# Performance work log

Hardware: AMD Instinct MI355X
Metric: run time of the kernel (lower is better)

## Reference

```python
import jax, jax.numpy as jnp
import numpy as np

TWO_PI = 6.283185307179586


def setup_inputs() -> dict:
    key = jax.random.key(0)
    k1, k2, k3, k4, k5, k6 = jax.random.split(key, 6)
    B, T, D = 2, 8192, 1024
    x = jax.random.normal(k1, (B, T, D), dtype=jnp.float32)
    # nn.Linear weights are [out, in]; init with small scale like torch default
    s = 1.0 / np.sqrt(D)
    Wk = jax.random.uniform(k2, (D, D), jnp.float32, -s, s)
    Wv = jax.random.uniform(k3, (D, D), jnp.float32, -s, s)
    Wo = jax.random.uniform(k4, (D, D), jnp.float32, -s, s)
    # random phasor frequencies in [0, 2*pi)
    freqs = jax.random.uniform(k5, (D,), jnp.float32, 0.0, TWO_PI)
    return {"x": x, "Wk": Wk, "Wv": Wv, "Wo": Wo, "freqs": freqs}


def reference(x, Wk, Wv, Wo, freqs):
    B, T, C = x.shape
    # k projection is computed in the original forward but never used downstream
    k_real = x @ Wk.T  # [B,T,D] (dead value, kept for fidelity)
    v_real = x @ Wv.T  # [B,T,D]
    v = v_real.astype(jnp.complex64)
    # rotors: per-position unit phasors exp(i * t * freqs), shape [T, D]
    t = jnp.arange(T, dtype=jnp.float32)
    rotors = jnp.exp(1j * (t[:, None] * freqs[None, :])).astype(jnp.complex64)
    # bind each value with its rotor and accumulate causally (O(N) memory trace)
    memory_trace = jnp.cumsum(v * rotors[None, :, :], axis=1)  # [B,T,D] complex64
    # retrieve by unbinding with the conjugate rotor; take the real component
    retrieved = jnp.real(memory_trace * jnp.conj(rotors)[None, :, :])  # [B,T,D]
    return retrieved @ Wo.T
```

## Files before the change

kernel.cpp:

```cpp
#include <hip/hip_runtime.h>
#include <hip/hip_bf16.h>


#define B_  2
#define T_  8192
#define D_  1024
#define BT_ 16384
#define CS_ 64
#define NCHUNK_ 128

typedef __attribute__((ext_vector_type(4))) float f32x4;
typedef __attribute__((ext_vector_type(8))) short bf16x8;

static __device__ inline unsigned short f2bf(float f) {
    union { float f; unsigned int u; } a;
    a.f = f;
    unsigned int u = a.u;
    return (unsigned short)((u + 0x7FFFu + ((u >> 16) & 1u)) >> 16);
}
static __device__ inline float bf2f(unsigned short h) {
    union { unsigned int u; float f; } a;
    a.u = ((unsigned int)h) << 16;
    return a.f;
}

__global__ __launch_bounds__(256) void cast_all(const float* __restrict__ x,
                                                const float* __restrict__ Wv,
                                                const float* __restrict__ Wo,
                                                unsigned short* __restrict__ xb,
                                                unsigned short* __restrict__ wvb,
                                                unsigned short* __restrict__ wob) {
    const int nx = BT_ * D_ / 4;
    const int nw = D_ * D_ / 4;
    int i = blockIdx.x * 256 + threadIdx.x;
    const float4* src;
    unsigned short* dst;
    int j;
    if (i < nx)            { src = (const float4*)x;  dst = xb;  j = i; }
    else if (i < nx + nw)  { src = (const float4*)Wv; dst = wvb; j = i - nx; }
    else                   { src = (const float4*)Wo; dst = wob; j = i - nx - nw; }
    float4 v = src[j];
    ushort4 o;
    o.x = f2bf(v.x); o.y = f2bf(v.y); o.z = f2bf(v.z); o.w = f2bf(v.w);
    ((ushort4*)dst)[j] = o;
}

template <bool BF16OUT, bool FUSE_SUMS>
__global__ __launch_bounds__(512, 2) void gemm_bt(const short* __restrict__ A,
                                                  const short* __restrict__ Bm,
                                                  void* __restrict__ Cout,
                                                  const float* __restrict__ freqs,
                                                  float* __restrict__ csum,
                                                  int M, int N, int K) {
    __shared__ short lds[65536];
    const int tid = threadIdx.x;
    const int lane = tid & 63;
    const int wave = tid >> 6;
    const int wm = wave >> 2, wn = wave & 3;

    const int nb = N >> 8;
    const int id = blockIdx.x;
    const int xcd = id & 7;
    const int slot = id >> 3;
    const int bn = (slot % nb) * 256;
    const int bm = (xcd * ((M >> 8) >> 3) + slot / nb) * 256;

    const int srow = lane >> 3;
    const int sg = lane & 7;
    const short* gsrc[8];
#pragma unroll
    for (int c = 0; c < 4; ++c) {
        const int r = c * 64 + wave * 8 + srow;
        const int col = (sg ^ (r & 7)) * 8;
        gsrc[c]     = A  + (size_t)(bm + r) * K + col;
        gsrc[c + 4] = Bm + (size_t)(bn + r) * K + col;
    }

    auto stage = [&](int kt, int sl) {
        const int koff = kt * 64;
        short* dstA = &lds[sl * 32768 + wave * 512];
        short* dstB = &lds[sl * 32768 + 16384 + wave * 512];
#pragma unroll
        for (int c = 0; c < 4; ++c) {
            __builtin_amdgcn_global_load_lds(
                (const __attribute__((address_space(1))) void*)(gsrc[c] + koff),
                (__attribute__((address_space(3))) void*)(dstA + c * 4096), 16, 0, 0);
            __builtin_amdgcn_global_load_lds(
                (const __attribute__((address_space(1))) void*)(gsrc[c + 4] + koff),
                (__attribute__((address_space(3))) void*)(dstB + c * 4096), 16, 0, 0);
        }
    };

    const int c4r = lane >> 4;
    int aoff[8][2], boff[4][2];
#pragma unroll
    for (int i = 0; i < 8; ++i) {
        const int m = wm * 128 + i * 16 + (lane & 15);
#pragma unroll
        for (int ks = 0; ks < 2; ++ks)
            aoff[i][ks] = m * 64 + (((ks * 4 + c4r) ^ (m & 7)) * 8);
    }
#pragma unroll
    for (int j = 0; j < 4; ++j) {
        const int n = wn * 64 + j * 16 + (lane & 15);
#pragma unroll
        for (int ks = 0; ks < 2; ++ks)
            boff[j][ks] = 16384 + n * 64 + (((ks * 4 + c4r) ^ (n & 7)) * 8);
    }

    f32x4 acc[8][4] = {};

    stage(0, 0);
    stage(1, 1);

    const int NT = K >> 6;
#pragma unroll 1
    for (int t = 0; t < NT; ++t) {
        if (t < NT - 1) asm volatile("s_waitcnt vmcnt(8)" ::: "memory");
        else            asm volatile("s_waitcnt vmcnt(0)" ::: "memory");
        __builtin_amdgcn_sched_barrier(0);
        __builtin_amdgcn_s_barrier();
        __builtin_amdgcn_sched_barrier(0);

        const int sb = (t & 1) * 32768;
#pragma unroll
        for (int ks = 0; ks < 2; ++ks) {
            bf16x8 bb[4];
#pragma unroll
            for (int j = 0; j < 4; ++j)
                bb[j] = *(const bf16x8*)&lds[sb + boff[j][ks]];
#pragma unroll
            for (int ih = 0; ih < 2; ++ih) {
                bf16x8 aa[4];
#pragma unroll
                for (int ii = 0; ii < 4; ++ii)
                    aa[ii] = *(const bf16x8*)&lds[sb + aoff[ih * 4 + ii][ks]];
                __builtin_amdgcn_s_setprio(1);
#pragma unroll
                for (int ii = 0; ii < 4; ++ii)
#pragma unroll
                    for (int j = 0; j < 4; ++j)
                        acc[ih * 4 + ii][j] = __builtin_amdgcn_mfma_f32_16x16x32_bf16(
                            aa[ii], bb[j], acc[ih * 4 + ii][j], 0, 0, 0);
                __builtin_amdgcn_s_setprio(0);
            }
        }
        asm volatile("s_waitcnt lgkmcnt(0)" ::: "memory");
        __builtin_amdgcn_sched_barrier(0);
        __builtin_amdgcn_s_barrier();
        __builtin_amdgcn_sched_barrier(0);
        if (t < NT - 2) stage(t + 2, t & 1);
    }

    const int row0 = c4r * 4;
#pragma unroll
    for (int i = 0; i < 8; ++i) {
#pragma unroll
        for (int j = 0; j < 4; ++j) {
            const int col = bn + wn * 64 + j * 16 + (lane & 15);
#pragma unroll
            for (int r = 0; r < 4; ++r) {
                const size_t row = (size_t)bm + wm * 128 + i * 16 + row0 + r;
                if constexpr (BF16OUT)
                    ((unsigned short*)Cout)[row * N + col] = f2bf(acc[i][j][r]);
                else
                    ((float*)Cout)[row * N + col] = acc[i][j][r];
            }
        }
    }

    if constexpr (FUSE_SUMS) {
        const int b = bm >> 13;
        const int trow = bm & 8191;
#pragma unroll
        for (int ig = 0; ig < 2; ++ig) {
            const int chunk = (trow >> 6) + wm * 2 + ig;
            const int t0 = trow + wm * 128 + ig * 64 + c4r * 4;
#pragma unroll
            for (int j = 0; j < 4; ++j) {
                const int d = bn + wn * 64 + j * 16 + (lane & 15);
                const float f = freqs[d];
                float ss, cc2;
                sincosf((float)t0 * f, &ss, &cc2);
                float s1, c1;
                sincosf(f, &s1, &c1);
                float c2 = c1 * c1 - s1 * s1, s2 = 2.f * c1 * s1;
                float c4 = c2 * c2 - s2 * s2, s4 = 2.f * c2 * s2;
                float c8 = c4 * c4 - s4 * s4, s8 = 2.f * c4 * s4;
                float c12 = c8 * c4 - s8 * s4, s12 = s8 * c4 + c8 * s4;
                float c13 = c12 * c1 - s12 * s1, s13 = s12 * c1 + c12 * s1;
                float ar = 0.f, ai = 0.f;
                float cr = cc2, sr2 = ss;
#pragma unroll
                for (int ii = 0; ii < 4; ++ii) {
                    const int i = ig * 4 + ii;
#pragma unroll
                    for (int r = 0; r < 4; ++r) {
                        const float w = acc[i][j][r];
                        ar = fmaf(w, cr, ar); ai = fmaf(w, sr2, ai);
                        const float ec = (r < 3) ? c1 : c13;
                        const float es = (r < 3) ? s1 : s13;
                        const float nc = cr * ec - sr2 * es;
                        const float ns = sr2 * ec + cr * es;
                        cr = nc; sr2 = ns;
                    }
                }
                ar += __shfl_xor(ar, 16); ai += __shfl_xor(ai, 16);
                ar += __shfl_xor(ar, 32); ai += __shfl_xor(ai, 32);
                if (c4r == 0)
                    *(float2*)(csum + (((size_t)b * NCHUNK_ + chunk) * D_ + d) * 2) =
                        make_float2(ar, ai);
            }
        }
    }
}

__global__ __launch_bounds__(256) void scan_pass2(float* __restrict__ csum) {
    const int g = blockIdx.x * 256 + threadIdx.x;
    const int b = g / D_;
    const int d = g % D_;
    float2* cs = (float2*)csum;
    const size_t base = (size_t)b * NCHUNK_ * D_ + d;
    float pr = 0.f, pi = 0.f;
    for (int cc = 0; cc < NCHUNK_; cc += 32) {
        float2 buf[32];
#pragma unroll
        for (int k = 0; k < 32; ++k) buf[k] = cs[base + (size_t)(cc + k) * D_];
#pragma unroll
        for (int k = 0; k < 32; ++k) {
            float r = buf[k].x, im = buf[k].y;
            buf[k] = make_float2(pr, pi);
            pr += r; pi += im;
        }
#pragma unroll
        for (int k = 0; k < 32; ++k) cs[base + (size_t)(cc + k) * D_] = buf[k];
    }
}

__global__ __launch_bounds__(256) void scan_pass3(const unsigned short* __restrict__ v,
                                                  const float* __restrict__ freqs,
                                                  const float* __restrict__ csum,
                                                  unsigned short* __restrict__ ret) {
    const int chunk = blockIdx.x;
    const int d0 = blockIdx.y * 512 + threadIdx.x * 2;
    const int b = blockIdx.z;

    float fr[2], s[2], c[2], sf[2], cf[2], ar[2], ai[2];
    {
        float2 f2 = *(const float2*)(freqs + d0);
        fr[0] = f2.x; fr[1] = f2.y;
    }
    const float t0f = (float)(chunk * CS_);
#pragma unroll
    for (int k = 0; k < 2; ++k) {
        sincosf(t0f * fr[k], &s[k], &c[k]);
        sincosf(fr[k], &sf[k], &cf[k]);
    }
    {
        const float4 o = *(const float4*)(csum + (((size_t)b * NCHUNK_ + chunk) * D_ + d0) * 2);
        ar[0] = o.x; ai[0] = o.y; ar[1] = o.z; ai[1] = o.w;
    }
    const unsigned int* vp = (const unsigned int*)(v + ((size_t)b * T_ + chunk * CS_) * D_ + d0);
    unsigned int* rp = (unsigned int*)(ret + ((size_t)b * T_ + chunk * CS_) * D_ + d0);
    for (int tb = 0; tb < CS_; tb += 8) {
        unsigned int w[8];
#pragma unroll
        for (int u = 0; u < 8; ++u) w[u] = vp[(size_t)(tb + u) * (D_ / 2)];
#pragma unroll
        for (int u = 0; u < 8; ++u) {
            float wv[2], o[2];
            wv[0] = bf2f((unsigned short)w[u]);
            wv[1] = bf2f((unsigned short)(w[u] >> 16));
#pragma unroll
            for (int k = 0; k < 2; ++k) {
                ar[k] = fmaf(wv[k], c[k], ar[k]);
                ai[k] = fmaf(wv[k], s[k], ai[k]);
                o[k] = ar[k] * c[k] + ai[k] * s[k];
                float nc = c[k] * cf[k] - s[k] * sf[k];
                float ns = s[k] * cf[k] + c[k] * sf[k];
                c[k] = nc; s[k] = ns;
            }
            rp[(size_t)(tb + u) * (D_ / 2)] =
                (unsigned int)f2bf(o[0]) | ((unsigned int)f2bf(o[1]) << 16);
        }
    }
}

extern "C" void kernel_launch(void* const* d_in, const int* in_sizes, int n_in,
                              void* d_out, int out_size, void* d_ws, size_t ws_size,
                              hipStream_t stream) {
    const float* x     = (const float*)d_in[0];
    const float* Wv    = (const float*)d_in[2];
    const float* Wo    = (const float*)d_in[3];
    const float* freqs = (const float*)d_in[4];
    float* out = (float*)d_out;

    char* ws = (char*)d_ws;
    unsigned short* x_bf  = (unsigned short*)ws;
    unsigned short* Wv_bf = (unsigned short*)(ws + 33554432);
    unsigned short* Wo_bf = (unsigned short*)(ws + 35651584);
    unsigned short* ret   = (unsigned short*)(ws + 37748736);
    float*          csum  = (float*)(ws + 71303168);
    unsigned short* v_bf = (unsigned short*)d_out;

    cast_all<<<(BT_ * D_ / 4 + 2 * D_ * D_ / 4) / 256, 256, 0, stream>>>(
        x, Wv, Wo, x_bf, Wv_bf, Wo_bf);

    gemm_bt<true, true><<<(BT_ / 256) * (D_ / 256), 512, 0, stream>>>(
        (const short*)x_bf, (const short*)Wv_bf, (void*)v_bf, freqs, csum, BT_, D_, D_);

    scan_pass2<<<(B_ * D_) / 256, 256, 0, stream>>>(csum);
    dim3 p3grid(NCHUNK_, D_ / 512, B_);
    scan_pass3<<<p3grid, 256, 0, stream>>>(v_bf, freqs, csum, ret);

    gemm_bt<false, false><<<(BT_ / 256) * (D_ / 256), 512, 0, stream>>>(
        (const short*)ret, (const short*)Wo_bf, (void*)out, nullptr, nullptr, BT_, D_, D_);
}
```

Before: 234.2 us.

## Split GEMM main loop into four quadrant phases with interleaved async loads

Restructures the bf16 MFMA GEMM main loop into four quadrant sub-phases. Each phase loads a subset of A/B fragments from LDS, issues a few global-to-LDS loads for future tiles, and runs 16 MFMAs. This spreads global loads across the iteration and overlaps LDS reads with MFMA work, instead of one big compute block followed by a batched stage. It also simplifies the address math with precomputed swizzle offsets, at the cost of more barriers per iteration and tricky buffer-reuse ordering.

```diff
diff --git a/kernel.cpp b/kernel.cpp
--- a/kernel.cpp
+++ b/kernel.cpp
@@ -67,89 +67,126 @@
 
     const int srow = lane >> 3;
     const int sg = lane & 7;
-    const short* gsrc[8];
-#pragma unroll
-    for (int c = 0; c < 4; ++c) {
-        const int r = c * 64 + wave * 8 + srow;
-        const int col = (sg ^ (r & 7)) * 8;
-        gsrc[c]     = A  + (size_t)(bm + r) * K + col;
-        gsrc[c + 4] = Bm + (size_t)(bn + r) * K + col;
-    }
-
-    auto stage = [&](int kt, int sl) {
-        const int koff = kt * 64;
-        short* dstA = &lds[sl * 32768 + wave * 512];
-        short* dstB = &lds[sl * 32768 + 16384 + wave * 512];
-#pragma unroll
-        for (int c = 0; c < 4; ++c) {
-            __builtin_amdgcn_global_load_lds(
-                (const __attribute__((address_space(1))) void*)(gsrc[c] + koff),
-                (__attribute__((address_space(3))) void*)(dstA + c * 4096), 16, 0, 0);
-            __builtin_amdgcn_global_load_lds(
-                (const __attribute__((address_space(1))) void*)(gsrc[c + 4] + koff),
-                (__attribute__((address_space(3))) void*)(dstB + c * 4096), 16, 0, 0);
-        }
+    const size_t cstep = (size_t)64 * K;
+    const short* gA = A + (size_t)(bm + wave * 8 + srow) * K + ((sg ^ srow) * 8);
+    const short* gB = Bm + (size_t)(bn + wave * 8 + srow) * K + ((sg ^ srow) * 8);
+
+    auto stage1 = [&](int kt, int g) {
+        const int c = g & 3;
+        const short* src = ((g & 4) ? gB : gA) + c * cstep + kt * 64;
+        short* dst = &lds[(kt & 1) * 32768 + ((g & 4) ? 16384 : 0) + c * 4096 + wave * 512];
+        __builtin_amdgcn_global_load_lds(
+            (const __attribute__((address_space(1))) void*)src,
+            (__attribute__((address_space(3))) void*)dst, 16, 0, 0);
     };
 
+    const int l15 = lane & 15;
     const int c4r = lane >> 4;
-    int aoff[8][2], boff[4][2];
-#pragma unroll
-    for (int i = 0; i < 8; ++i) {
-        const int m = wm * 128 + i * 16 + (lane & 15);
-#pragma unroll
-        for (int ks = 0; ks < 2; ++ks)
-            aoff[i][ks] = m * 64 + (((ks * 4 + c4r) ^ (m & 7)) * 8);
-    }
-#pragma unroll
-    for (int j = 0; j < 4; ++j) {
-        const int n = wn * 64 + j * 16 + (lane & 15);
-#pragma unroll
-        for (int ks = 0; ks < 2; ++ks)
-            boff[j][ks] = 16384 + n * 64 + (((ks * 4 + c4r) ^ (n & 7)) * 8);
-    }
+    const int swz0 = ((c4r) ^ (lane & 7)) * 8;
+    const int swz1 = ((4 + c4r) ^ (lane & 7)) * 8;
+    const int abase = (wm * 128 + l15) * 64;
+    const int bbase = 16384 + (wn * 64 + l15) * 64;
 
     f32x4 acc[8][4] = {};
 
-    stage(0, 0);
-    stage(1, 1);
+    stage1(0, 0); stage1(0, 1); stage1(0, 2); stage1(0, 3);
+    stage1(0, 4); stage1(0, 5); stage1(0, 6); stage1(0, 7);
+    stage1(1, 0); stage1(1, 2);
+    stage1(1, 4); stage1(1, 5); stage1(1, 6); stage1(1, 7);
+    asm volatile("s_waitcnt vmcnt(6)" ::: "memory");
+    __builtin_amdgcn_sched_barrier(0);
+    __builtin_amdgcn_s_barrier();
 
     const int NT = K >> 6;
 #pragma unroll 1
     for (int t = 0; t < NT; ++t) {
-        if (t < NT - 1) asm volatile("s_waitcnt vmcnt(8)" ::: "memory");
+        const int sb = (t & 1) * 32768;
+        bf16x8 av[4][2], b01[2][2], b23[2][2];
+
+#pragma unroll
+        for (int ii = 0; ii < 4; ++ii) {
+            av[ii][0] = *(const bf16x8*)&lds[sb + abase + ii * 1024 + swz0];
+            av[ii][1] = *(const bf16x8*)&lds[sb + abase + ii * 1024 + swz1];
+        }
+#pragma unroll
+        for (int j = 0; j < 2; ++j) {
+            b01[j][0] = *(const bf16x8*)&lds[sb + bbase + j * 1024 + swz0];
+            b01[j][1] = *(const bf16x8*)&lds[sb + bbase + j * 1024 + swz1];
+        }
+        if (t + 1 < NT) { stage1(t + 1, 1); stage1(t + 1, 3); }
+        __builtin_amdgcn_s_barrier();
+        asm volatile("s_waitcnt lgkmcnt(0)" ::: "memory");
+        __builtin_amdgcn_sched_barrier(0);
+        __builtin_amdgcn_s_setprio(1);
+#pragma unroll
+        for (int ks = 0; ks < 2; ++ks)
+#pragma unroll
+            for (int ii = 0; ii < 4; ++ii)
+#pragma unroll
+                for (int j = 0; j < 2; ++j)
+                    acc[ii][j] = __builtin_amdgcn_mfma_f32_16x16x32_bf16(
+                        av[ii][ks], b01[j][ks], acc[ii][j], 0, 0, 0);
+        __builtin_amdgcn_s_setprio(0);
+        __builtin_amdgcn_s_barrier();
+
+#pragma unroll
+        for (int j = 0; j < 2; ++j) {
+            b23[j][0] = *(const bf16x8*)&lds[sb + bbase + (2 + j) * 1024 + swz0];
+            b23[j][1] = *(const bf16x8*)&lds[sb + bbase + (2 + j) * 1024 + swz1];
+        }
+        if (t + 2 < NT) { stage1(t + 2, 0); stage1(t + 2, 2); }
+        __builtin_amdgcn_s_barrier();
+        asm volatile("s_waitcnt lgkmcnt(0)" ::: "memory");
+        __builtin_amdgcn_sched_barrier(0);
+        __builtin_amdgcn_s_setprio(1);
+#pragma unroll
+        for (int ks = 0; ks < 2; ++ks)
+#pragma unroll
+            for (int ii = 0; ii < 4; ++ii)
+#pragma unroll
+                for (int j = 0; j < 2; ++j)
+                    acc[ii][2 + j] = __builtin_amdgcn_mfma_f32_16x16x32_bf16(
+                        av[ii][ks], b23[j][ks], acc[ii][2 + j], 0, 0, 0);
+        __builtin_amdgcn_s_setprio(0);
+        __builtin_amdgcn_s_barrier();
+
+#pragma unroll
+        for (int ii = 0; ii < 4; ++ii) {
+            av[ii][0] = *(const bf16x8*)&lds[sb + abase + (4 + ii) * 1024 + swz0];
+            av[ii][1] = *(const bf16x8*)&lds[sb + abase + (4 + ii) * 1024 + swz1];
+        }
+        if (t + 2 < NT) { stage1(t + 2, 4); stage1(t + 2, 5); }
+        __builtin_amdgcn_s_barrier();
+        asm volatile("s_waitcnt lgkmcnt(0)" ::: "memory");
+        __builtin_amdgcn_sched_barrier(0);
+        __builtin_amdgcn_s_setprio(1);
+#pragma unroll
+        for (int ks = 0; ks < 2; ++ks)
+#pragma unroll
+            for (int ii = 0; ii < 4; ++ii)
+#pragma unroll
+                for (int j = 0; j < 2; ++j)
+                    acc[4 + ii][2 + j] = __builtin_amdgcn_mfma_f32_16x16x32_bf16(
+                        av[ii][ks], b23[j][ks], acc[4 + ii][2 + j], 0, 0, 0);
+        __builtin_amdgcn_s_setprio(0);
+        __builtin_amdgcn_s_barrier();
+
+        if (t + 2 < NT) { stage1(t + 2, 6); stage1(t + 2, 7); }
+        if (t + 2 < NT) asm volatile("s_waitcnt vmcnt(6)" ::: "memory");
         else            asm volatile("s_waitcnt vmcnt(0)" ::: "memory");
         __builtin_amdgcn_sched_barrier(0);
         __builtin_amdgcn_s_barrier();
-        __builtin_amdgcn_sched_barrier(0);
-
-        const int sb = (t & 1) * 32768;
-#pragma unroll
-        for (int ks = 0; ks < 2; ++ks) {
-            bf16x8 bb[4];
-#pragma unroll
-            for (int j = 0; j < 4; ++j)
-                bb[j] = *(const bf16x8*)&lds[sb + boff[j][ks]];
-#pragma unroll
-            for (int ih = 0; ih < 2; ++ih) {
-                bf16x8 aa[4];
-#pragma unroll
-                for (int ii = 0; ii < 4; ++ii)
-                    aa[ii] = *(const bf16x8*)&lds[sb + aoff[ih * 4 + ii][ks]];
-                __builtin_amdgcn_s_setprio(1);
-#pragma unroll
-                for (int ii = 0; ii < 4; ++ii)
-#pragma unroll
-                    for (int j = 0; j < 4; ++j)
-                        acc[ih * 4 + ii][j] = __builtin_amdgcn_mfma_f32_16x16x32_bf16(
-                            aa[ii], bb[j], acc[ih * 4 + ii][j], 0, 0, 0);
-                __builtin_amdgcn_s_setprio(0);
-            }
-        }
-        asm volatile("s_waitcnt lgkmcnt(0)" ::: "memory");
-        __builtin_amdgcn_sched_barrier(0);
-        __builtin_amdgcn_s_barrier();
-        __builtin_amdgcn_sched_barrier(0);
-        if (t < NT - 2) stage(t + 2, t & 1);
+        __builtin_amdgcn_s_setprio(1);
+#pragma unroll
+        for (int ks = 0; ks < 2; ++ks)
+#pragma unroll
+            for (int ii = 0; ii < 4; ++ii)
+#pragma unroll
+                for (int j = 0; j < 2; ++j)
+                    acc[4 + ii][j] = __builtin_amdgcn_mfma_f32_16x16x32_bf16(
+                        av[ii][ks], b01[j][ks], acc[4 + ii][j], 0, 0, 0);
+        __builtin_amdgcn_s_setprio(0);
+        __builtin_amdgcn_s_barrier();
     }
 
     const int row0 = c4r * 4;
```

After: 235.0 us. About the same (+0.3%).
